# Performance work log

Hardware: AMD Instinct MI355X
Metric: run time of the kernel (lower is better)

The kernel has to match this reference:

```python
import jax, jax.numpy as jnp
import numpy as np

B, N, D = 256, 512, 64  # batch, positions, channels; units = spatial_units = D


def setup_inputs() -> dict:
    key = jax.random.key(0)
    ks = jax.random.split(key, 9)
    g = 1.0 / np.sqrt(D)  # glorot-ish scale for square matrices
    return {
        "x": jax.random.normal(ks[0], (B, N, D), dtype=jnp.float32),
        "Wq_t": jax.random.normal(ks[1], (D, D), dtype=jnp.float32) * g,
        "Wk_t": jax.random.normal(ks[2], (D, D), dtype=jnp.float32) * g,
        "Wv_t": jax.random.normal(ks[3], (D, D), dtype=jnp.float32) * g,
        "Wq_s": jax.random.normal(ks[4], (D, D), dtype=jnp.float32) * g,
        "Wk_s": jax.random.normal(ks[5], (D, D), dtype=jnp.float32) * g,
        "Wv_s": jax.random.normal(ks[6], (D, D), dtype=jnp.float32) * g,
        "Wd_t": jax.random.normal(ks[7], (D, D), dtype=jnp.float32) * g,
        "bd_t": jnp.zeros((D,), dtype=jnp.float32),
        "Wd_s": jax.random.normal(ks[8], (D, D), dtype=jnp.float32) * g,
        "bd_s": jnp.zeros((D,), dtype=jnp.float32),
    }


def _branch(x, Wq, Wk, Wv, Wd, bd):
    # x: [B, N, D]; one self-attention branch followed by a Dense layer.
    q = jnp.einsum("bnd,de->bne", x, Wq)
    k = jnp.einsum("bnd,de->bne", x, Wk)
    v = jnp.einsum("bnd,de->bne", x, Wv)
    scale = 1.0 / jnp.sqrt(jnp.asarray(Wk.shape[-1], dtype=x.dtype))
    scores = jnp.einsum("bne,bme->bnm", q, k) * scale  # [B, N, N]
    w = jax.nn.softmax(scores, axis=-1)
    attn = jnp.einsum("bnm,bmd->bnd", w, v)
    return jnp.einsum("bnd,de->bne", attn, Wd) + bd


def reference(x, Wq_t, Wk_t, Wv_t, Wq_s, Wk_s, Wv_s, Wd_t, bd_t, Wd_s, bd_s):
    temporal = _branch(x, Wq_t, Wk_t, Wv_t, Wd_t, bd_t)
    spatial = _branch(x, Wq_s, Wk_s, Wv_s, Wd_s, bd_s)
    gate = jax.nn.sigmoid(temporal + spatial)
    return x * gate
```

## Files before the change

### kernel.cpp

```cpp
#include <hip/hip_runtime.h>

typedef __attribute__((ext_vector_type(8))) short short8;
typedef __attribute__((ext_vector_type(4))) short short4v;
typedef __attribute__((ext_vector_type(4))) float float4v;

#define MFMA16(a, b, c) __builtin_amdgcn_mfma_f32_16x16x32_bf16((a), (b), (c), 0, 0, 0)

constexpr int kThreads = 512;
constexpr int LDS_TOTAL_BYTES = 163840;

static __device__ __forceinline__ unsigned short f2bf(float f) {
  unsigned int u = __float_as_uint(f);
  u = (u + 0x7fffu + ((u >> 16) & 1u)) >> 16;
  return (unsigned short)u;
}

static __device__ __forceinline__ int wsw_idx(int e, int d) {
  return ((((d >> 3) << 9) + (e << 3) + (d & 7)) ^ (((d >> 3) & 3) << 3));
}

__global__ __launch_bounds__(kThreads, 2) void ts_attn_fused(
    const float* __restrict__ x, const float* __restrict__ Wq_t,
    const float* __restrict__ Wk_t, const float* __restrict__ Wv_t,
    const float* __restrict__ Wq_s, const float* __restrict__ Wk_s,
    const float* __restrict__ Wv_s, const float* __restrict__ Wd_t,
    const float* __restrict__ bd_t, const float* __restrict__ Wd_s,
    const float* __restrict__ bd_s, float* __restrict__ out,
    unsigned short* __restrict__ qws) {
  extern __shared__ __align__(16) unsigned short smem[];
  unsigned short* Ksw = smem;
  unsigned short* Vsw = smem + 32768;
  unsigned short* Wst = smem + 65536;
  unsigned short* Wdsw = smem + 77824;

  const int tid = threadIdx.x;
  const int wv = tid >> 6;
  const int lane = tid & 63;
  const int ln = lane & 15;
  const int quad = lane >> 4;
  const int e8 = ln & 7;
  const int b = blockIdx.x;

  const float* xb = x + (size_t)b * (512 * 64);
  float* outb = out + (size_t)b * (512 * 64);
  unsigned short* qg = qws + (size_t)b * (512 * 64);

  float4v bd4[4];
#pragma unroll
  for (int nt = 0; nt < 4; ++nt) {
    const float4v bt = *reinterpret_cast<const float4v*>(bd_t + nt * 16 + quad * 4);
    const float4v bs = *reinterpret_cast<const float4v*>(bd_s + nt * 16 + quad * 4);
    bd4[nt] = bt + bs;
  }

#pragma unroll 1
  for (int br = 0; br < 2; ++br) {
    const float* Wq = br ? Wq_s : Wq_t;
    const float* Wk = br ? Wk_s : Wk_t;
    const float* Wv = br ? Wv_s : Wv_t;
    const float* Wd = br ? Wd_s : Wd_t;

    {
      const int d = tid >> 3;
      const int e0 = (tid & 7) * 8;
      const float* srcs[3] = {Wq, Wk, Wv};
#pragma unroll
      for (int g = 0; g < 3; ++g) {
        const float4v u = *reinterpret_cast<const float4v*>(srcs[g] + d * 64 + e0);
        const float4v v = *reinterpret_cast<const float4v*>(srcs[g] + d * 64 + e0 + 4);
        unsigned short* dst = Wst + g * 4096;
#pragma unroll
        for (int i = 0; i < 4; ++i) dst[wsw_idx(e0 + i, d)] = f2bf(u[i]);
#pragma unroll
        for (int i = 0; i < 4; ++i) dst[wsw_idx(e0 + 4 + i, d)] = f2bf(v[i]);
      }
      const int cp_ = d >> 5;
      const int c = d & 31;
      const int qd_ = (c >> 2) & 3;
      const int h_ = ((c >> 4) << 2) | (c & 3);
      const int gbase = (cp_ * 4 + qd_);
      const float4v u = *reinterpret_cast<const float4v*>(Wd + d * 64 + e0);
      const float4v v = *reinterpret_cast<const float4v*>(Wd + d * 64 + e0 + 4);
#pragma unroll
      for (int i = 0; i < 4; ++i) {
        const int e = e0 + i;
        Wdsw[e * 64 + ((gbase ^ (e & 7)) << 3) + h_] = f2bf(u[i]);
      }
#pragma unroll
      for (int i = 0; i < 4; ++i) {
        const int e = e0 + 4 + i;
        Wdsw[e * 64 + ((gbase ^ (e & 7)) << 3) + h_] = f2bf(v[i]);
      }
    }
    __syncthreads();

#pragma unroll 1
    for (int mi = 0; mi < 4; ++mi) {
      const int mrow = (wv + mi * 8) * 16 + ln;
      const int kpq = mrow >> 5;
      const int w5 = mrow & 31;
      const int jj = ((w5 >> 4) << 2) | (w5 & 3);
      const int qg2 = (w5 >> 2) & 3;
      short8 xa0, xa1;
      {
        const float4v u0 = *reinterpret_cast<const float4v*>(xb + mrow * 64 + quad * 8);
        const float4v v0 = *reinterpret_cast<const float4v*>(xb + mrow * 64 + quad * 8 + 4);
        const float4v u1 = *reinterpret_cast<const float4v*>(xb + mrow * 64 + 32 + quad * 8);
        const float4v v1 = *reinterpret_cast<const float4v*>(xb + mrow * 64 + 32 + quad * 8 + 4);
#pragma unroll
        for (int i = 0; i < 4; ++i) {
          xa0[i] = (short)f2bf(u0[i]);
          xa0[4 + i] = (short)f2bf(v0[i]);
          xa1[i] = (short)f2bf(u1[i]);
          xa1[4 + i] = (short)f2bf(v1[i]);
        }
      }
#pragma unroll
      for (int g = 0; g < 3; ++g) {
        const unsigned short* Wg = Wst + g * 4096;
#pragma unroll
        for (int nt = 0; nt < 4; ++nt) {
          const short8 w0 = *reinterpret_cast<const short8*>(Wg + wsw_idx(nt * 16 + ln, quad * 8));
          const short8 w1 = *reinterpret_cast<const short8*>(Wg + wsw_idx(nt * 16 + ln, 32 + quad * 8));
          float4v acc = {0.f, 0.f, 0.f, 0.f};
          acc = MFMA16(w0, xa0, acc);
          acc = MFMA16(w1, xa1, acc);
          if (g == 0) {
            short4v pk;
#pragma unroll
            for (int r = 0; r < 4; ++r) pk[r] = (short)f2bf(acc[r]);
            *reinterpret_cast<short4v*>(
                qg + mrow * 64 + (nt >> 1) * 32 + quad * 8 + (nt & 1) * 4) = pk;
          } else if (g == 1) {
            short4v pk;
#pragma unroll
            for (int r = 0; r < 4; ++r) pk[r] = (short)f2bf(acc[r]);
            const int gswz = ((nt >> 1) * 4 + quad) ^ (mrow & 7);
            *reinterpret_cast<short4v*>(
                Ksw + mrow * 64 + (gswz << 3) + (nt & 1) * 4) = pk;
          } else {
#pragma unroll
            for (int r = 0; r < 4; ++r) {
              const int d = nt * 16 + quad * 4 + r;
              Vsw[(d << 9) + (qg2 << 7) + ((kpq ^ (d & 7)) << 3) + jj] = f2bf(acc[r]);
            }
          }
        }
      }
    }
    __syncthreads();

#pragma unroll 1
    for (int qi = 0; qi < 4; ++qi) {
      const int qt = wv + qi * 8;
      const unsigned short* qrow = qg + (qt * 16 + ln) * 64;
      const short8 qa = *reinterpret_cast<const short8*>(qrow + quad * 8);
      const short8 qb = *reinterpret_cast<const short8*>(qrow + 32 + quad * 8);

      const int kb0 = ln * 64 + ((quad ^ e8) << 3);
      const int kb1 = ln * 64 + (((4 + quad) ^ e8) << 3);
      const int e88 = e8 * 8;

      float4v o[4];
#pragma unroll
      for (int i = 0; i < 4; ++i) o[i] = (float4v){0.f, 0.f, 0.f, 0.f};
      float mrun = -3.0e38f;
      float sum = 0.f;

#pragma unroll 1
      for (int ch = 0; ch < 4; ++ch) {
        float4v s[8];
#pragma unroll
        for (int k8 = 0; k8 < 8; ++k8) {
          const int kt = ch * 8 + k8;
          const short8 k0 = *reinterpret_cast<const short8*>(Ksw + kt * 1024 + kb0);
          const short8 k1 = *reinterpret_cast<const short8*>(Ksw + kt * 1024 + kb1);
          float4v acc = {0.f, 0.f, 0.f, 0.f};
          acc = MFMA16(k0, qa, acc);
          acc = MFMA16(k1, qb, acc);
          s[k8] = acc;
        }

        float4v m4 = s[0];
#pragma unroll
        for (int k8 = 1; k8 < 8; ++k8)
#pragma unroll
          for (int r = 0; r < 4; ++r) m4[r] = fmaxf(m4[r], s[k8][r]);
        float cmx = fmaxf(fmaxf(m4[0], m4[1]), fmaxf(m4[2], m4[3]));
        cmx = fmaxf(cmx, __shfl_xor(cmx, 16, 64));
        cmx = fmaxf(cmx, __shfl_xor(cmx, 32, 64));

        const float mnew = fmaxf(mrun, cmx);
        const float scale = __expf((mrun - mnew) * 0.125f);
        sum *= scale;
#pragma unroll
        for (int i = 0; i < 4; ++i)
#pragma unroll
          for (int r = 0; r < 4; ++r) o[i][r] *= scale;
        const float offs = -mnew * 0.125f;
        mrun = mnew;

#pragma unroll
        for (int kp = 0; kp < 4; ++kp) {
          float p[8];
#pragma unroll
          for (int h = 0; h < 2; ++h) {
            const int k8 = kp * 2 + h;
#pragma unroll
            for (int r = 0; r < 4; ++r)
              p[h * 4 + r] = __expf(fmaf(s[k8][r], 0.125f, offs));
          }
          sum += ((p[0] + p[4]) + (p[1] + p[5])) + ((p[2] + p[6]) + (p[3] + p[7]));
          short8 pf;
#pragma unroll
          for (int j = 0; j < 8; ++j) pf[j] = (short)f2bf(p[j]);
          const int kpg = ch * 4 + kp;
#pragma unroll
          for (int nto = 0; nto < 4; ++nto) {
            const int vb = (nto * 16 + ln) * 512 + quad * 128;
            const short8 vf = *reinterpret_cast<const short8*>(Vsw + vb + ((kpg * 8) ^ e88));
            o[nto] = MFMA16(vf, pf, o[nto]);
          }
        }
      }

      sum += __shfl_xor(sum, 16, 64);
      sum += __shfl_xor(sum, 32, 64);
      const float inv = 1.0f / sum;

      short8 of0, of1;
#pragma unroll
      for (int r = 0; r < 4; ++r) {
        of0[r] = (short)f2bf(o[0][r] * inv);
        of0[4 + r] = (short)f2bf(o[1][r] * inv);
        of1[r] = (short)f2bf(o[2][r] * inv);
        of1[4 + r] = (short)f2bf(o[3][r] * inv);
      }

#pragma unroll
      for (int nt = 0; nt < 4; ++nt) {
        const int ebase = (nt * 16 + ln) * 64;
        const short8 w0 = *reinterpret_cast<const short8*>(
            Wdsw + ebase + ((quad ^ e8) << 3));
        const short8 w1 = *reinterpret_cast<const short8*>(
            Wdsw + ebase + (((4 + quad) ^ e8) << 3));
        float4v acc = {0.f, 0.f, 0.f, 0.f};
        acc = MFMA16(w0, of0, acc);
        acc = MFMA16(w1, of1, acc);
        const int row = qt * 16 + ln;
        const int e0 = nt * 16 + quad * 4;
        float4v* op = reinterpret_cast<float4v*>(outb + row * 64 + e0);
        if (br == 0) {
          *op = acc;
        } else {
          const float4v parked = *op;
          const float4v xv = *reinterpret_cast<const float4v*>(xb + row * 64 + e0);
          float4v res;
#pragma unroll
          for (int r = 0; r < 4; ++r) {
            const float z = parked[r] + acc[r] + bd4[nt][r];
            const float gate = 1.0f / (1.0f + __expf(-z));
            res[r] = xv[r] * gate;
          }
          *op = res;
        }
      }
    }
    __syncthreads();
  }
}

extern "C" void kernel_launch(void* const* d_in, const int* in_sizes, int n_in,
                              void* d_out, int out_size, void* d_ws, size_t ws_size,
                              hipStream_t stream) {
  const float* x = (const float*)d_in[0];
  const float* Wq_t = (const float*)d_in[1];
  const float* Wk_t = (const float*)d_in[2];
  const float* Wv_t = (const float*)d_in[3];
  const float* Wq_s = (const float*)d_in[4];
  const float* Wk_s = (const float*)d_in[5];
  const float* Wv_s = (const float*)d_in[6];
  const float* Wd_t = (const float*)d_in[7];
  const float* bd_t = (const float*)d_in[8];
  const float* Wd_s = (const float*)d_in[9];
  const float* bd_s = (const float*)d_in[10];
  float* out = (float*)d_out;
  unsigned short* qws = (unsigned short*)d_ws;

  hipFuncSetAttribute(reinterpret_cast<const void*>(ts_attn_fused),
                      hipFuncAttributeMaxDynamicSharedMemorySize, LDS_TOTAL_BYTES);
  ts_attn_fused<<<dim3(256), dim3(kThreads), LDS_TOTAL_BYTES, stream>>>(
      x, Wq_t, Wk_t, Wv_t, Wq_s, Wk_s, Wv_s, Wd_t, bd_t, Wd_s, bd_s, out, qws);
}
```

Before: 180.5 us.

## Process two query tiles per wave to share K/V LDS fragment loads

Each wave now handles two 16-row query tiles at once, so every K and V fragment read from LDS feeds two MFMAs instead of one. The aim is to halve LDS traffic per unit of attention work and give the scheduler independent MFMA chains to interleave. The V swizzle also gains an extra XOR with the key-group index to change the bank mapping of V reads. The cost is roughly doubled accumulator and score register use, which may hurt occupancy under the two-blocks-per-CU launch bound or cause spills.

```diff
diff --git a/kernel.cpp b/kernel.cpp
--- a/kernel.cpp
+++ b/kernel.cpp
@@ -142,7 +142,8 @@
 #pragma unroll
             for (int r = 0; r < 4; ++r) {
               const int d = nt * 16 + quad * 4 + r;
-              Vsw[(d << 9) + (qg2 << 7) + ((kpq ^ (d & 7)) << 3) + jj] = f2bf(acc[r]);
+              const int gv = (kpq ^ (d & 7) ^ qg2);
+              Vsw[(d << 9) + (qg2 << 7) + (gv << 3) + jj] = f2bf(acc[r]);
             }
           }
         }
@@ -151,90 +152,130 @@
     __syncthreads();
 
 #pragma unroll 1
-    for (int qi = 0; qi < 4; ++qi) {
-      const int qt = wv + qi * 8;
-      const unsigned short* qrow = qg + (qt * 16 + ln) * 64;
-      const short8 qa = *reinterpret_cast<const short8*>(qrow + quad * 8);
-      const short8 qb = *reinterpret_cast<const short8*>(qrow + 32 + quad * 8);
+    for (int qi = 0; qi < 2; ++qi) {
+      const int qtA = wv + qi * 16;
+      const int qtB = wv + 8 + qi * 16;
+      const unsigned short* qrowA = qg + (qtA * 16 + ln) * 64;
+      const unsigned short* qrowB = qg + (qtB * 16 + ln) * 64;
+      const short8 qaA = *reinterpret_cast<const short8*>(qrowA + quad * 8);
+      const short8 qbA = *reinterpret_cast<const short8*>(qrowA + 32 + quad * 8);
+      const short8 qaB = *reinterpret_cast<const short8*>(qrowB + quad * 8);
+      const short8 qbB = *reinterpret_cast<const short8*>(qrowB + 32 + quad * 8);
 
       const int kb0 = ln * 64 + ((quad ^ e8) << 3);
       const int kb1 = ln * 64 + (((4 + quad) ^ e8) << 3);
-      const int e88 = e8 * 8;
-
-      float4v o[4];
-#pragma unroll
-      for (int i = 0; i < 4; ++i) o[i] = (float4v){0.f, 0.f, 0.f, 0.f};
-      float mrun = -3.0e38f;
-      float sum = 0.f;
+      const int vxor = (quad << 3) ^ (e8 << 3);
+
+      float4v oA[4], oB[4];
+#pragma unroll
+      for (int i = 0; i < 4; ++i) {
+        oA[i] = (float4v){0.f, 0.f, 0.f, 0.f};
+        oB[i] = (float4v){0.f, 0.f, 0.f, 0.f};
+      }
+      float mrunA = -3.0e38f, mrunB = -3.0e38f;
+      float sumA = 0.f, sumB = 0.f;
 
 #pragma unroll 1
       for (int ch = 0; ch < 4; ++ch) {
-        float4v s[8];
+        float4v sA[8], sB[8];
 #pragma unroll
         for (int k8 = 0; k8 < 8; ++k8) {
           const int kt = ch * 8 + k8;
           const short8 k0 = *reinterpret_cast<const short8*>(Ksw + kt * 1024 + kb0);
           const short8 k1 = *reinterpret_cast<const short8*>(Ksw + kt * 1024 + kb1);
-          float4v acc = {0.f, 0.f, 0.f, 0.f};
-          acc = MFMA16(k0, qa, acc);
-          acc = MFMA16(k1, qb, acc);
-          s[k8] = acc;
-        }
-
-        float4v m4 = s[0];
+          float4v aA = {0.f, 0.f, 0.f, 0.f};
+          aA = MFMA16(k0, qaA, aA);
+          aA = MFMA16(k1, qbA, aA);
+          sA[k8] = aA;
+          float4v aB = {0.f, 0.f, 0.f, 0.f};
+          aB = MFMA16(k0, qaB, aB);
+          aB = MFMA16(k1, qbB, aB);
+          sB[k8] = aB;
+        }
+
+        float4v m4A = sA[0], m4B = sB[0];
 #pragma unroll
         for (int k8 = 1; k8 < 8; ++k8)
 #pragma unroll
-          for (int r = 0; r < 4; ++r) m4[r] = fmaxf(m4[r], s[k8][r]);
-        float cmx = fmaxf(fmaxf(m4[0], m4[1]), fmaxf(m4[2], m4[3]));
-        cmx = fmaxf(cmx, __shfl_xor(cmx, 16, 64));
-        cmx = fmaxf(cmx, __shfl_xor(cmx, 32, 64));
-
-        const float mnew = fmaxf(mrun, cmx);
-        const float scale = __expf((mrun - mnew) * 0.125f);
-        sum *= scale;
+          for (int r = 0; r < 4; ++r) {
+            m4A[r] = fmaxf(m4A[r], sA[k8][r]);
+            m4B[r] = fmaxf(m4B[r], sB[k8][r]);
+          }
+        float cmxA = fmaxf(fmaxf(m4A[0], m4A[1]), fmaxf(m4A[2], m4A[3]));
+        float cmxB = fmaxf(fmaxf(m4B[0], m4B[1]), fmaxf(m4B[2], m4B[3]));
+        cmxA = fmaxf(cmxA, __shfl_xor(cmxA, 16, 64));
+        cmxB = fmaxf(cmxB, __shfl_xor(cmxB, 16, 64));
+        cmxA = fmaxf(cmxA, __shfl_xor(cmxA, 32, 64));
+        cmxB = fmaxf(cmxB, __shfl_xor(cmxB, 32, 64));
+
+        const float mnewA = fmaxf(mrunA, cmxA);
+        const float mnewB = fmaxf(mrunB, cmxB);
+        const float scaleA = __expf((mrunA - mnewA) * 0.125f);
+        const float scaleB = __expf((mrunB - mnewB) * 0.125f);
+        sumA *= scaleA;
+        sumB *= scaleB;
 #pragma unroll
         for (int i = 0; i < 4; ++i)
 #pragma unroll
-          for (int r = 0; r < 4; ++r) o[i][r] *= scale;
-        const float offs = -mnew * 0.125f;
-        mrun = mnew;
+          for (int r = 0; r < 4; ++r) {
+            oA[i][r] *= scaleA;
+            oB[i][r] *= scaleB;
+          }
+        const float offsA = -mnewA * 0.125f;
+        const float offsB = -mnewB * 0.125f;
+        mrunA = mnewA;
+        mrunB = mnewB;
 
 #pragma unroll
         for (int kp = 0; kp < 4; ++kp) {
-          float p[8];
+          float pA[8], pB[8];
 #pragma unroll
           for (int h = 0; h < 2; ++h) {
             const int k8 = kp * 2 + h;
 #pragma unroll
-            for (int r = 0; r < 4; ++r)
-              p[h * 4 + r] = __expf(fmaf(s[k8][r], 0.125f, offs));
-          }
-          sum += ((p[0] + p[4]) + (p[1] + p[5])) + ((p[2] + p[6]) + (p[3] + p[7]));
-          short8 pf;
-#pragma unroll
-          for (int j = 0; j < 8; ++j) pf[j] = (short)f2bf(p[j]);
+            for (int r = 0; r < 4; ++r) {
+              pA[h * 4 + r] = __expf(fmaf(sA[k8][r], 0.125f, offsA));
+              pB[h * 4 + r] = __expf(fmaf(sB[k8][r], 0.125f, offsB));
+            }
+          }
+          sumA += ((pA[0] + pA[4]) + (pA[1] + pA[5])) + ((pA[2] + pA[6]) + (pA[3] + pA[7]));
+          sumB += ((pB[0] + pB[4]) + (pB[1] + pB[5])) + ((pB[2] + pB[6]) + (pB[3] + pB[7]));
+          short8 pfA, pfB;
+#pragma unroll
+          for (int j = 0; j < 8; ++j) {
+            pfA[j] = (short)f2bf(pA[j]);
+            pfB[j] = (short)f2bf(pB[j]);
+          }
           const int kpg = ch * 4 + kp;
 #pragma unroll
           for (int nto = 0; nto < 4; ++nto) {
             const int vb = (nto * 16 + ln) * 512 + quad * 128;
-            const short8 vf = *reinterpret_cast<const short8*>(Vsw + vb + ((kpg * 8) ^ e88));
-            o[nto] = MFMA16(vf, pf, o[nto]);
-          }
-        }
-      }
-
-      sum += __shfl_xor(sum, 16, 64);
-      sum += __shfl_xor(sum, 32, 64);
-      const float inv = 1.0f / sum;
-
-      short8 of0, of1;
+            const short8 vf = *reinterpret_cast<const short8*>(
+                Vsw + vb + (((kpg << 3) ^ vxor)));
+            oA[nto] = MFMA16(vf, pfA, oA[nto]);
+            oB[nto] = MFMA16(vf, pfB, oB[nto]);
+          }
+        }
+      }
+
+      sumA += __shfl_xor(sumA, 16, 64);
+      sumB += __shfl_xor(sumB, 16, 64);
+      sumA += __shfl_xor(sumA, 32, 64);
+      sumB += __shfl_xor(sumB, 32, 64);
+      const float invA = 1.0f / sumA;
+      const float invB = 1.0f / sumB;
+
+      short8 of0A, of1A, of0B, of1B;
 #pragma unroll
       for (int r = 0; r < 4; ++r) {
-        of0[r] = (short)f2bf(o[0][r] * inv);
-        of0[4 + r] = (short)f2bf(o[1][r] * inv);
-        of1[r] = (short)f2bf(o[2][r] * inv);
-        of1[4 + r] = (short)f2bf(o[3][r] * inv);
+        of0A[r] = (short)f2bf(oA[0][r] * invA);
+        of0A[4 + r] = (short)f2bf(oA[1][r] * invA);
+        of1A[r] = (short)f2bf(oA[2][r] * invA);
+        of1A[4 + r] = (short)f2bf(oA[3][r] * invA);
+        of0B[r] = (short)f2bf(oB[0][r] * invB);
+        of0B[4 + r] = (short)f2bf(oB[1][r] * invB);
+        of1B[r] = (short)f2bf(oB[2][r] * invB);
+        of1B[4 + r] = (short)f2bf(oB[3][r] * invB);
       }
 
 #pragma unroll
@@ -244,25 +285,32 @@
             Wdsw + ebase + ((quad ^ e8) << 3));
         const short8 w1 = *reinterpret_cast<const short8*>(
             Wdsw + ebase + (((4 + quad) ^ e8) << 3));
-        float4v acc = {0.f, 0.f, 0.f, 0.f};
-        acc = MFMA16(w0, of0, acc);
-        acc = MFMA16(w1, of1, acc);
-        const int row = qt * 16 + ln;
+        float4v accA = {0.f, 0.f, 0.f, 0.f};
+        accA = MFMA16(w0, of0A, accA);
+        accA = MFMA16(w1, of1A, accA);
+        float4v accB = {0.f, 0.f, 0.f, 0.f};
+        accB = MFMA16(w0, of0B, accB);
+        accB = MFMA16(w1, of1B, accB);
         const int e0 = nt * 16 + quad * 4;
-        float4v* op = reinterpret_cast<float4v*>(outb + row * 64 + e0);
-        if (br == 0) {
-          *op = acc;
-        } else {
-          const float4v parked = *op;
-          const float4v xv = *reinterpret_cast<const float4v*>(xb + row * 64 + e0);
-          float4v res;
-#pragma unroll
-          for (int r = 0; r < 4; ++r) {
-            const float z = parked[r] + acc[r] + bd4[nt][r];
-            const float gate = 1.0f / (1.0f + __expf(-z));
-            res[r] = xv[r] * gate;
-          }
-          *op = res;
+#pragma unroll
+        for (int t = 0; t < 2; ++t) {
+          const int row = (t == 0 ? qtA : qtB) * 16 + ln;
+          const float4v acc = t == 0 ? accA : accB;
+          float4v* op = reinterpret_cast<float4v*>(outb + row * 64 + e0);
+          if (br == 0) {
+            *op = acc;
+          } else {
+            const float4v parked = *op;
+            const float4v xv = *reinterpret_cast<const float4v*>(xb + row * 64 + e0);
+            float4v res;
+#pragma unroll
+            for (int r = 0; r < 4; ++r) {
+              const float z = parked[r] + acc[r] + bd4[nt][r];
+              const float gate = 1.0f / (1.0f + __expf(-z));
+              res[r] = xv[r] * gate;
+            }
+            *op = res;
+          }
         }
       }
     }
```

New measurement: 200.4 us. +11.0%, slower.

## Use 1024-thread blocks, smaller softmax chunks, and re-swizzled V layout

Applied to the files above, without the earlier changes.

Doubles the block to 1024 threads (16 waves) and halves each wave's share of projection rows and query tiles, while shrinking the online-softmax chunk from 8 to 4 key tiles to cut register pressure. It adds an extra XOR on qg2 to the V LDS swizzle, meant to reduce bank conflicts, and switches bf16 conversion to the native cast. Bias loads move into the epilogue instead of being held in registers. The goal is more waves per CU to hide MFMA/LDS latency; the risks are losing two-blocks-per-CU residency and doing more softmax rescale steps.

```diff
diff --git a/kernel.cpp b/kernel.cpp
--- a/kernel.cpp
+++ b/kernel.cpp
@@ -6,20 +6,19 @@
 
 #define MFMA16(a, b, c) __builtin_amdgcn_mfma_f32_16x16x32_bf16((a), (b), (c), 0, 0, 0)
 
-constexpr int kThreads = 512;
+constexpr int kThreads = 1024;
 constexpr int LDS_TOTAL_BYTES = 163840;
 
 static __device__ __forceinline__ unsigned short f2bf(float f) {
-  unsigned int u = __float_as_uint(f);
-  u = (u + 0x7fffu + ((u >> 16) & 1u)) >> 16;
-  return (unsigned short)u;
+  __bf16 h = (__bf16)f;
+  return __builtin_bit_cast(unsigned short, h);
 }
 
 static __device__ __forceinline__ int wsw_idx(int e, int d) {
   return ((((d >> 3) << 9) + (e << 3) + (d & 7)) ^ (((d >> 3) & 3) << 3));
 }
 
-__global__ __launch_bounds__(kThreads, 2) void ts_attn_fused(
+__global__ __launch_bounds__(kThreads) void ts_attn_fused(
     const float* __restrict__ x, const float* __restrict__ Wq_t,
     const float* __restrict__ Wk_t, const float* __restrict__ Wv_t,
     const float* __restrict__ Wq_s, const float* __restrict__ Wk_s,
@@ -45,14 +44,6 @@
   float* outb = out + (size_t)b * (512 * 64);
   unsigned short* qg = qws + (size_t)b * (512 * 64);
 
-  float4v bd4[4];
-#pragma unroll
-  for (int nt = 0; nt < 4; ++nt) {
-    const float4v bt = *reinterpret_cast<const float4v*>(bd_t + nt * 16 + quad * 4);
-    const float4v bs = *reinterpret_cast<const float4v*>(bd_s + nt * 16 + quad * 4);
-    bd4[nt] = bt + bs;
-  }
-
 #pragma unroll 1
   for (int br = 0; br < 2; ++br) {
     const float* Wq = br ? Wq_s : Wq_t;
@@ -61,18 +52,15 @@
     const float* Wd = br ? Wd_s : Wd_t;
 
     {
-      const int d = tid >> 3;
-      const int e0 = (tid & 7) * 8;
+      const int d = tid >> 4;
+      const int e0 = (tid & 15) * 4;
       const float* srcs[3] = {Wq, Wk, Wv};
 #pragma unroll
       for (int g = 0; g < 3; ++g) {
         const float4v u = *reinterpret_cast<const float4v*>(srcs[g] + d * 64 + e0);
-        const float4v v = *reinterpret_cast<const float4v*>(srcs[g] + d * 64 + e0 + 4);
         unsigned short* dst = Wst + g * 4096;
 #pragma unroll
         for (int i = 0; i < 4; ++i) dst[wsw_idx(e0 + i, d)] = f2bf(u[i]);
-#pragma unroll
-        for (int i = 0; i < 4; ++i) dst[wsw_idx(e0 + 4 + i, d)] = f2bf(v[i]);
       }
       const int cp_ = d >> 5;
       const int c = d & 31;
@@ -80,23 +68,17 @@
       const int h_ = ((c >> 4) << 2) | (c & 3);
       const int gbase = (cp_ * 4 + qd_);
       const float4v u = *reinterpret_cast<const float4v*>(Wd + d * 64 + e0);
-      const float4v v = *reinterpret_cast<const float4v*>(Wd + d * 64 + e0 + 4);
 #pragma unroll
       for (int i = 0; i < 4; ++i) {
         const int e = e0 + i;
         Wdsw[e * 64 + ((gbase ^ (e & 7)) << 3) + h_] = f2bf(u[i]);
       }
-#pragma unroll
-      for (int i = 0; i < 4; ++i) {
-        const int e = e0 + 4 + i;
-        Wdsw[e * 64 + ((gbase ^ (e & 7)) << 3) + h_] = f2bf(v[i]);
-      }
     }
     __syncthreads();
 
 #pragma unroll 1
-    for (int mi = 0; mi < 4; ++mi) {
-      const int mrow = (wv + mi * 8) * 16 + ln;
+    for (int mi = 0; mi < 2; ++mi) {
+      const int mrow = (wv + mi * 16) * 16 + ln;
       const int kpq = mrow >> 5;
       const int w5 = mrow & 31;
       const int jj = ((w5 >> 4) << 2) | (w5 & 3);
@@ -142,7 +124,8 @@
 #pragma unroll
             for (int r = 0; r < 4; ++r) {
               const int d = nt * 16 + quad * 4 + r;
-              Vsw[(d << 9) + (qg2 << 7) + ((kpq ^ (d & 7)) << 3) + jj] = f2bf(acc[r]);
+              const int gv = (kpq ^ (d & 7) ^ qg2);
+              Vsw[(d << 9) + (qg2 << 7) + (gv << 3) + jj] = f2bf(acc[r]);
             }
           }
         }
@@ -150,119 +133,124 @@
     }
     __syncthreads();
 
-#pragma unroll 1
-    for (int qi = 0; qi < 4; ++qi) {
-      const int qt = wv + qi * 8;
-      const unsigned short* qrow = qg + (qt * 16 + ln) * 64;
-      const short8 qa = *reinterpret_cast<const short8*>(qrow + quad * 8);
-      const short8 qb = *reinterpret_cast<const short8*>(qrow + 32 + quad * 8);
-
+    {
       const int kb0 = ln * 64 + ((quad ^ e8) << 3);
       const int kb1 = ln * 64 + (((4 + quad) ^ e8) << 3);
-      const int e88 = e8 * 8;
-
-      float4v o[4];
-#pragma unroll
-      for (int i = 0; i < 4; ++i) o[i] = (float4v){0.f, 0.f, 0.f, 0.f};
-      float mrun = -3.0e38f;
-      float sum = 0.f;
-
-#pragma unroll 1
-      for (int ch = 0; ch < 4; ++ch) {
-        float4v s[8];
-#pragma unroll
-        for (int k8 = 0; k8 < 8; ++k8) {
-          const int kt = ch * 8 + k8;
-          const short8 k0 = *reinterpret_cast<const short8*>(Ksw + kt * 1024 + kb0);
-          const short8 k1 = *reinterpret_cast<const short8*>(Ksw + kt * 1024 + kb1);
+      const int vxor = (quad << 3) ^ (e8 << 3);
+
+#pragma unroll 1
+      for (int qi = 0; qi < 2; ++qi) {
+        const int qt = wv + qi * 16;
+        const unsigned short* qrow = qg + (qt * 16 + ln) * 64;
+        const short8 qa = *reinterpret_cast<const short8*>(qrow + quad * 8);
+        const short8 qb = *reinterpret_cast<const short8*>(qrow + 32 + quad * 8);
+
+        float4v o[4];
+#pragma unroll
+        for (int i = 0; i < 4; ++i) o[i] = (float4v){0.f, 0.f, 0.f, 0.f};
+        float mrun = -3.0e38f;
+        float sum = 0.f;
+
+#pragma unroll 1
+        for (int ch = 0; ch < 8; ++ch) {
+          float4v s[4];
+#pragma unroll
+          for (int k8 = 0; k8 < 4; ++k8) {
+            const int kt = ch * 4 + k8;
+            const short8 k0 = *reinterpret_cast<const short8*>(Ksw + kt * 1024 + kb0);
+            const short8 k1 = *reinterpret_cast<const short8*>(Ksw + kt * 1024 + kb1);
+            float4v a = {0.f, 0.f, 0.f, 0.f};
+            a = MFMA16(k0, qa, a);
+            a = MFMA16(k1, qb, a);
+            s[k8] = a;
+          }
+
+          float4v m4 = s[0];
+#pragma unroll
+          for (int k8 = 1; k8 < 4; ++k8)
+#pragma unroll
+            for (int r = 0; r < 4; ++r) m4[r] = fmaxf(m4[r], s[k8][r]);
+          float cmx = fmaxf(fmaxf(m4[0], m4[1]), fmaxf(m4[2], m4[3]));
+          cmx = fmaxf(cmx, __shfl_xor(cmx, 16, 64));
+          cmx = fmaxf(cmx, __shfl_xor(cmx, 32, 64));
+
+          const float mnew = fmaxf(mrun, cmx);
+          const float scale = __expf((mrun - mnew) * 0.125f);
+          sum *= scale;
+#pragma unroll
+          for (int i = 0; i < 4; ++i)
+#pragma unroll
+            for (int r = 0; r < 4; ++r) o[i][r] *= scale;
+          const float offs = -mnew * 0.125f;
+          mrun = mnew;
+
+#pragma unroll
+          for (int kp = 0; kp < 2; ++kp) {
+            float p[8];
+#pragma unroll
+            for (int h = 0; h < 2; ++h) {
+              const int k8 = kp * 2 + h;
+#pragma unroll
+              for (int r = 0; r < 4; ++r)
+                p[h * 4 + r] = __expf(fmaf(s[k8][r], 0.125f, offs));
+            }
+            sum += ((p[0] + p[4]) + (p[1] + p[5])) + ((p[2] + p[6]) + (p[3] + p[7]));
+            short8 pf;
+#pragma unroll
+            for (int j = 0; j < 8; ++j) pf[j] = (short)f2bf(p[j]);
+            const int kpg = ch * 2 + kp;
+#pragma unroll
+            for (int nto = 0; nto < 4; ++nto) {
+              const int vb = (nto * 16 + ln) * 512 + quad * 128;
+              const short8 vf = *reinterpret_cast<const short8*>(
+                  Vsw + vb + (((kpg << 3) ^ vxor)));
+              o[nto] = MFMA16(vf, pf, o[nto]);
+            }
+          }
+        }
+
+        sum += __shfl_xor(sum, 16, 64);
+        sum += __shfl_xor(sum, 32, 64);
+        const float inv = 1.0f / sum;
+
+        short8 of0, of1;
+#pragma unroll
+        for (int r = 0; r < 4; ++r) {
+          of0[r] = (short)f2bf(o[0][r] * inv);
+          of0[4 + r] = (short)f2bf(o[1][r] * inv);
+          of1[r] = (short)f2bf(o[2][r] * inv);
+          of1[4 + r] = (short)f2bf(o[3][r] * inv);
+        }
+
+#pragma unroll
+        for (int nt = 0; nt < 4; ++nt) {
+          const int ebase = (nt * 16 + ln) * 64;
+          const short8 w0 = *reinterpret_cast<const short8*>(
+              Wdsw + ebase + ((quad ^ e8) << 3));
+          const short8 w1 = *reinterpret_cast<const short8*>(
+              Wdsw + ebase + (((4 + quad) ^ e8) << 3));
           float4v acc = {0.f, 0.f, 0.f, 0.f};
-          acc = MFMA16(k0, qa, acc);
-          acc = MFMA16(k1, qb, acc);
-          s[k8] = acc;
-        }
-
-        float4v m4 = s[0];
-#pragma unroll
-        for (int k8 = 1; k8 < 8; ++k8)
-#pragma unroll
-          for (int r = 0; r < 4; ++r) m4[r] = fmaxf(m4[r], s[k8][r]);
-        float cmx = fmaxf(fmaxf(m4[0], m4[1]), fmaxf(m4[2], m4[3]));
-        cmx = fmaxf(cmx, __shfl_xor(cmx, 16, 64));
-        cmx = fmaxf(cmx, __shfl_xor(cmx, 32, 64));
-
-        const float mnew = fmaxf(mrun, cmx);
-        const float scale = __expf((mrun - mnew) * 0.125f);
-        sum *= scale;
-#pragma unroll
-        for (int i = 0; i < 4; ++i)
-#pragma unroll
-          for (int r = 0; r < 4; ++r) o[i][r] *= scale;
-        const float offs = -mnew * 0.125f;
-        mrun = mnew;
-
-#pragma unroll
-        for (int kp = 0; kp < 4; ++kp) {
-          float p[8];
-#pragma unroll
-          for (int h = 0; h < 2; ++h) {
-            const int k8 = kp * 2 + h;
-#pragma unroll
-            for (int r = 0; r < 4; ++r)
-              p[h * 4 + r] = __expf(fmaf(s[k8][r], 0.125f, offs));
-          }
-          sum += ((p[0] + p[4]) + (p[1] + p[5])) + ((p[2] + p[6]) + (p[3] + p[7]));
-          short8 pf;
-#pragma unroll
-          for (int j = 0; j < 8; ++j) pf[j] = (short)f2bf(p[j]);
-          const int kpg = ch * 4 + kp;
-#pragma unroll
-          for (int nto = 0; nto < 4; ++nto) {
-            const int vb = (nto * 16 + ln) * 512 + quad * 128;
-            const short8 vf = *reinterpret_cast<const short8*>(Vsw + vb + ((kpg * 8) ^ e88));
-            o[nto] = MFMA16(vf, pf, o[nto]);
-          }
-        }
-      }
-
-      sum += __shfl_xor(sum, 16, 64);
-      sum += __shfl_xor(sum, 32, 64);
-      const float inv = 1.0f / sum;
-
-      short8 of0, of1;
-#pragma unroll
-      for (int r = 0; r < 4; ++r) {
-        of0[r] = (short)f2bf(o[0][r] * inv);
-        of0[4 + r] = (short)f2bf(o[1][r] * inv);
-        of1[r] = (short)f2bf(o[2][r] * inv);
-        of1[4 + r] = (short)f2bf(o[3][r] * inv);
-      }
-
-#pragma unroll
-      for (int nt = 0; nt < 4; ++nt) {
-        const int ebase = (nt * 16 + ln) * 64;
-        const short8 w0 = *reinterpret_cast<const short8*>(
-            Wdsw + ebase + ((quad ^ e8) << 3));
-        const short8 w1 = *reinterpret_cast<const short8*>(
-            Wdsw + ebase + (((4 + quad) ^ e8) << 3));
-        float4v acc = {0.f, 0.f, 0.f, 0.f};
-        acc = MFMA16(w0, of0, acc);
-        acc = MFMA16(w1, of1, acc);
-        const int row = qt * 16 + ln;
-        const int e0 = nt * 16 + quad * 4;
-        float4v* op = reinterpret_cast<float4v*>(outb + row * 64 + e0);
-        if (br == 0) {
-          *op = acc;
-        } else {
-          const float4v parked = *op;
-          const float4v xv = *reinterpret_cast<const float4v*>(xb + row * 64 + e0);
-          float4v res;
-#pragma unroll
-          for (int r = 0; r < 4; ++r) {
-            const float z = parked[r] + acc[r] + bd4[nt][r];
-            const float gate = 1.0f / (1.0f + __expf(-z));
-            res[r] = xv[r] * gate;
-          }
-          *op = res;
+          acc = MFMA16(w0, of0, acc);
+          acc = MFMA16(w1, of1, acc);
+          const int row = qt * 16 + ln;
+          const int e0 = nt * 16 + quad * 4;
+          float4v* op = reinterpret_cast<float4v*>(outb + row * 64 + e0);
+          if (br == 0) {
+            *op = acc;
+          } else {
+            const float4v bt = *reinterpret_cast<const float4v*>(bd_t + e0);
+            const float4v bs = *reinterpret_cast<const float4v*>(bd_s + e0);
+            const float4v parked = *op;
+            const float4v xv = *reinterpret_cast<const float4v*>(xb + row * 64 + e0);
+            float4v res;
+#pragma unroll
+            for (int r = 0; r < 4; ++r) {
+              const float z = parked[r] + acc[r] + bt[r] + bs[r];
+              const float gate = 1.0f / (1.0f + __expf(-z));
+              res[r] = xv[r] * gate;
+            }
+            *op = res;
+          }
         }
       }
     }
```

Result: slower. 236.9 us (+31.3%).
